# Kernel tuning notes

Hardware: AMD Instinct MI355X
Metric: run time of the kernel (lower is better)

Reference implementation:

```python
import jax, jax.numpy as jnp
import numpy as np

NUM_LAYERS = 3

def setup_inputs() -> dict:
    key = jax.random.key(0)
    ku, ki, ke1, ke2 = jax.random.split(key, 4)
    num_users, num_items, D, E = 100000, 50000, 128, 1000000
    # xavier-uniform-ish init scale for the embedding tables
    bound = float(np.sqrt(6.0 / (num_users + D)))
    user_w = jax.random.uniform(ku, (num_users, D), jnp.float32, -bound, bound)
    bound_i = float(np.sqrt(6.0 / (num_items + D)))
    item_w = jax.random.uniform(ki, (num_items, D), jnp.float32, -bound_i, bound_i)
    # bipartite edges: user -> item (item ids offset by num_users), plus reverse direction
    u = jax.random.randint(ke1, (E,), 0, num_users, dtype=jnp.int32)
    v = jax.random.randint(ke2, (E,), 0, num_items, dtype=jnp.int32) + num_users
    edge_index = jnp.stack([jnp.concatenate([u, v]), jnp.concatenate([v, u])])  # [2, 2E]
    return {"user_w": user_w, "item_w": item_w, "edge_index": edge_index,
            "num_users": num_users, "num_items": num_items}

def reference(user_w, item_w, edge_index, num_users, num_items):
    n_nodes = num_users + num_items
    src, dst = edge_index[0], edge_index[1]
    # degree via scatter-add (duplicate edges sum, same as coalesce)
    deg = jax.ops.segment_sum(jnp.ones_like(src, dtype=user_w.dtype), src,
                              num_segments=n_nodes)
    dinv = jnp.where(deg > 0, deg ** -0.5, 0.0)
    dinv = jnp.where(jnp.isfinite(dinv), dinv, 0.0)
    vals = dinv[src] * dinv[dst]  # normalized adjacency values, [2E]

    emb = jnp.concatenate([user_w, item_w], axis=0)  # [n_nodes, D]
    acc = emb
    x = emb
    for _ in range(NUM_LAYERS):
        # SpMM: out[s] += vals(e) * x[dst(e)]
        x = jax.ops.segment_sum(vals[:, None] * x[dst], src, num_segments=n_nodes)
        acc = acc + x
    final = acc / jnp.asarray(NUM_LAYERS + 1, dtype=emb.dtype)
    return final[:num_users], final[num_users:]
```

## Files before the change

kernel.cpp:

```cpp
#include <hip/hip_runtime.h>
#include <hip/hip_fp16.h>
#include <cstdint>
#include <cstddef>

#define D 128
#define BSH 9
#define BNODES 512
#define NBMAX 512
#define CCHUNK 8192
#define FP8_SCALE 2048.0f
#define FP8_INV_SCALE (1.0f / 2048.0f)

typedef float v2f __attribute__((ext_vector_type(2)));

static __device__ inline unsigned pack_fp8x4(float a, float b, float c, float d) {
    a = fminf(fmaxf(a, -440.f), 440.f);
    b = fminf(fmaxf(b, -440.f), 440.f);
    c = fminf(fmaxf(c, -440.f), 440.f);
    d = fminf(fmaxf(d, -440.f), 440.f);
    int r = 0;
    r = __builtin_amdgcn_cvt_pk_fp8_f32(a, b, r, false);
    r = __builtin_amdgcn_cvt_pk_fp8_f32(c, d, r, true);
    return (unsigned)r;
}


__global__ __launch_bounds__(256)
void k_hist_tohalf(const int* __restrict__ src, int* __restrict__ bhist,
                   int ne2, int nb, int nbh,
                   const float2* __restrict__ uw, const float2* __restrict__ iw,
                   __half2* __restrict__ x0, int nu2, int ntot2) {
    if ((int)blockIdx.x < nbh) {
        __shared__ int lc[NBMAX];
        for (int i = threadIdx.x; i < nb; i += 256) lc[i] = 0;
        __syncthreads();
        int base = blockIdx.x * CCHUNK;
        int lim = min(base + CCHUNK, ne2);
        for (int e = base + threadIdx.x; e < lim; e += 256)
            atomicAdd(&lc[src[e] >> BSH], 1);
        __syncthreads();
        for (int i = threadIdx.x; i < nb; i += 256)
            if (lc[i]) atomicAdd(&bhist[i], lc[i]);
    } else {
        int g = (blockIdx.x - nbh) * 256 + threadIdx.x;
        if (g < ntot2) {
            float2 v = (g < nu2) ? uw[g] : iw[g - nu2];
            x0[g] = __floats2half2_rn(v.x, v.y);
        }
    }
}

__global__ void k_bscan(const int* __restrict__ bhist, int* __restrict__ bbase,
                        int* __restrict__ bfill, int* __restrict__ rp,
                        int nb, int nn, int ne2) {
    __shared__ int a[NBMAX], b2[NBMAX];
    int t = threadIdx.x;
    int v = (t < nb) ? bhist[t] : 0;
    a[t] = v;
    __syncthreads();
    int* cur = a; int* nxt = b2;
    for (int o = 1; o < NBMAX; o <<= 1) {
        int x = cur[t];
        if (t >= o) x += cur[t - o];
        nxt[t] = x;
        __syncthreads();
        int* tm = cur; cur = nxt; nxt = tm;
    }
    int excl = cur[t] - v;
    if (t < nb) { bbase[t] = excl; bfill[t] = excl; }
    if (t == 0) { bbase[nb] = ne2; rp[nn] = ne2; }
}

__global__ __launch_bounds__(256)
void k_scatter(const int* __restrict__ src, const int* __restrict__ dst,
               int* __restrict__ bfill, int* __restrict__ tmp, int ne2, int nb) {
    __shared__ int lc[NBMAX], lb[NBMAX];
    for (int i = threadIdx.x; i < nb; i += 256) lc[i] = 0;
    __syncthreads();
    int base = blockIdx.x * CCHUNK;
    int rec[CCHUNK / 256];
#pragma unroll
    for (int i = 0; i < CCHUNK / 256; ++i) {
        int e = base + i * 256 + threadIdx.x;
        rec[i] = -1;
        if (e < ne2) {
            int b = src[e] >> BSH;
            int r = atomicAdd(&lc[b], 1);
            rec[i] = (r << BSH) | b;
        }
    }
    __syncthreads();
    for (int i = threadIdx.x; i < nb; i += 256)
        if (lc[i]) lb[i] = atomicAdd(&bfill[i], lc[i]);
    __syncthreads();
#pragma unroll
    for (int i = 0; i < CCHUNK / 256; ++i) {
        if (rec[i] >= 0) {
            int e = base + i * 256 + threadIdx.x;
            int b = rec[i] & (BNODES - 1);
            int r = rec[i] >> BSH;
            tmp[lb[b] + r] = ((src[e] & (BNODES - 1)) << 18) | dst[e];
        }
    }
}

__global__ __launch_bounds__(256)
void k_build(const int* __restrict__ tmp, const int* __restrict__ bbase,
             int* __restrict__ col, int* __restrict__ rp,
             float* __restrict__ dinv2, float* __restrict__ rinv,
             const float4* __restrict__ x0h, uint2* __restrict__ y0p, int nn) {
    __shared__ int cnt[BNODES];
    __shared__ int off[BNODES];
    __shared__ int wtot[4], woff[4];
    int bkt = blockIdx.x;
    int n0 = bkt << BSH;
    int nloc = min(BNODES, nn - n0);
    int ebeg = bbase[bkt], eend = bbase[bkt + 1];
    for (int i = threadIdx.x; i < BNODES; i += 256) cnt[i] = 0;
    __syncthreads();
    for (int e = ebeg + threadIdx.x; e < eend; e += 256)
        atomicAdd(&cnt[tmp[e] >> 18], 1);
    __syncthreads();
    int t = threadIdx.x;
    int c0 = cnt[2 * t], c1 = cnt[2 * t + 1];
    int s = c0 + c1;
    int lane = t & 63, wid = t >> 6;
    int x = s;
#pragma unroll
    for (int o = 1; o < 64; o <<= 1) {
        int y = __shfl_up(x, o);
        if (lane >= o) x += y;
    }
    if (lane == 63) wtot[wid] = x;
    __syncthreads();
    if (t == 0) { int a = 0; for (int k = 0; k < 4; ++k) { woff[k] = a; a += wtot[k]; } }
    __syncthreads();
    int eb = woff[wid] + x - s;
    off[2 * t] = eb;
    off[2 * t + 1] = eb + c0;
    __syncthreads();
    for (int i = threadIdx.x; i < nloc; i += 256) {
        rp[n0 + i] = ebeg + off[i];
        int c = cnt[i];
        float fc = (float)c;
        dinv2[n0 + i] = (c > 0) ? 1.0f / fc : 0.0f;
        rinv[n0 + i]  = (c > 0) ? sqrtf(fc) : 0.0f;
    }
    {
        int r = threadIdx.x >> 4;
        int l = threadIdx.x & 15;
        for (; r < nloc; r += 16) {
            int c = cnt[r];
            float sc = (c > 0) ? FP8_SCALE * rsqrtf((float)c) : 0.0f;
            float4 v = x0h[(size_t)(n0 + r) * 16 + l];
            const __half2* hp = reinterpret_cast<const __half2*>(&v);
            float2 f0 = __half22float2(hp[0]), f1 = __half22float2(hp[1]);
            float2 f2 = __half22float2(hp[2]), f3 = __half22float2(hp[3]);
            uint2 o;
            o.x = pack_fp8x4(sc * f0.x, sc * f0.y, sc * f1.x, sc * f1.y);
            o.y = pack_fp8x4(sc * f2.x, sc * f2.y, sc * f3.x, sc * f3.y);
            y0p[(size_t)(n0 + r) * 16 + l] = o;
        }
    }
    __syncthreads();
    for (int i = threadIdx.x; i < BNODES; i += 256) cnt[i] = 0;
    __syncthreads();
    for (int e = ebeg + threadIdx.x; e < eend; e += 256) {
        int v = tmp[e];
        int sl = v >> 18;
        int r = atomicAdd(&cnt[sl], 1);
        col[ebeg + off[sl] + r] = v & 0x3FFFF;
    }
}

template <int MODE>
__global__ __launch_bounds__(256)
void k_spmm(const uint2* __restrict__ yin, uint2* __restrict__ y8out,
            float4* __restrict__ h16out, const float4* __restrict__ aux1,
            const float4* __restrict__ aux2,
            const int* __restrict__ rp, const int* __restrict__ col,
            const float* __restrict__ dinv2, const float* __restrict__ rinv,
            float4* __restrict__ outp, int nn) {
    int wave = (blockIdx.x * blockDim.x + threadIdx.x) >> 6;
    int lane = threadIdx.x & 63;
    int g = lane >> 4, l16 = lane & 15;
    int node = wave * 4 + g;
    int beg = 0, end = 0;
    if (node < nn) { beg = rp[node]; end = rp[node + 1]; }
    v2f acc[4];
#pragma unroll
    for (int k = 0; k < 4; ++k) acc[k] = (v2f)(0.f);

    int srcl = g << 4;
    for (int base = beg; base < end; base += 16) {
        int p = base + l16;
        int d = (p < end) ? col[p] : 0;
        int m = min(16, end - base);
#pragma unroll 8
        for (int t = 0; t < m; ++t) {
            int dd = __shfl(d, srcl + t);
            uint2 u = yin[(size_t)dd * 16 + l16];
            acc[0] += __builtin_amdgcn_cvt_pk_f32_fp8((int)u.x, false);
            acc[1] += __builtin_amdgcn_cvt_pk_f32_fp8((int)u.x, true);
            acc[2] += __builtin_amdgcn_cvt_pk_f32_fp8((int)u.y, false);
            acc[3] += __builtin_amdgcn_cvt_pk_f32_fp8((int)u.y, true);
        }
    }
    if (node >= nn) return;
    float s2 = dinv2[node];
    size_t r16 = (size_t)node * 16 + l16;
    if (MODE != 2) {
        float yv[8];
#pragma unroll
        for (int k = 0; k < 4; ++k) {
            yv[2 * k]     = s2 * acc[k].x;
            yv[2 * k + 1] = s2 * acc[k].y;
        }
        uint2 o8;
        o8.x = pack_fp8x4(yv[0], yv[1], yv[2], yv[3]);
        o8.y = pack_fp8x4(yv[4], yv[5], yv[6], yv[7]);
        y8out[r16] = o8;
        if (MODE == 1) {
            float4 av = aux1[r16];
            const __half2* ap = reinterpret_cast<const __half2*>(&av);
#pragma unroll
            for (int k = 0; k < 4; ++k) {
                float2 fa = __half22float2(ap[k]);
                yv[2 * k]     += fa.x;
                yv[2 * k + 1] += fa.y;
            }
        }
        __half2 h[4];
#pragma unroll
        for (int k = 0; k < 4; ++k)
            h[k] = __floats2half2_rn(yv[2 * k], yv[2 * k + 1]);
        h16out[r16] = *reinterpret_cast<const float4*>(h);
    } else {
        float4 ev = aux1[r16];
        float4 zv = aux2[r16];
        const __half2* ep = reinterpret_cast<const __half2*>(&ev);
        const __half2* zp = reinterpret_cast<const __half2*>(&zv);
        float rs = rinv[node] * FP8_INV_SCALE;
        float o[8];
#pragma unroll
        for (int k = 0; k < 4; ++k) {
            float2 fe = __half22float2(ep[k]);
            float2 fz = __half22float2(zp[k]);
            o[2 * k]     = 0.25f * (fe.x + (fz.x + s2 * acc[k].x) * rs);
            o[2 * k + 1] = 0.25f * (fe.y + (fz.y + s2 * acc[k].y) * rs);
        }
        float4 w0 = make_float4(o[0], o[1], o[2], o[3]);
        float4 w1 = make_float4(o[4], o[5], o[6], o[7]);
        size_t r32 = (size_t)node * 32 + 2 * l16;
        outp[r32] = w0;
        outp[r32 + 1] = w1;
    }
}


extern "C" void kernel_launch(void* const* d_in, const int* in_sizes, int n_in,
                              void* d_out, int out_size, void* d_ws, size_t ws_size,
                              hipStream_t stream) {
    const float* uw = (const float*)d_in[0];
    const float* iw = (const float*)d_in[1];
    const int* ei = (const int*)d_in[2];

    const int NU = in_sizes[0] / D;
    const int NI = in_sizes[1] / D;
    const int NN = NU + NI;
    const int NE2 = in_sizes[2] / 2;
    const int* src = ei;
    const int* dst = ei + NE2;
    const int NB = (NN + BNODES - 1) >> BSH;

    char* p = (char*)d_ws;
    auto alloc = [&](size_t bytes) -> void* {
        void* r = (void*)p;
        p += (bytes + 255) & ~(size_t)255;
        return r;
    };
    int* bhist   = (int*)alloc(NBMAX * 4);
    int* bbase   = (int*)alloc((NBMAX + 1) * 4);
    int* bfill   = (int*)alloc(NBMAX * 4);
    int* rp      = (int*)alloc((size_t)(NN + 1) * 4);
    float* dinv2 = (float*)alloc((size_t)NN * 4);
    float* rinv  = (float*)alloc((size_t)NN * 4);
    int* col     = (int*)alloc((size_t)NE2 * 4);
    __half2* zh  = (__half2*)alloc((size_t)NN * D * 2);
    int* tmp     = (int*)zh;
    __half2* xa  = (__half2*)alloc((size_t)NN * D * 2);
    uint2* y0p   = (uint2*)alloc((size_t)NN * D);
    uint2* y1p   = (uint2*)alloc((size_t)NN * D);
    __half2* y1h = (__half2*)alloc((size_t)NN * D * 2);
    uint2* y2p   = y0p;
    float* outp  = (float*)d_out;

    hipMemsetAsync(bhist, 0, NBMAX * 4, stream);

    int ntot2 = NN * (D / 2);
    int nu2 = NU * (D / 2);
    int bce = (NE2 + CCHUNK - 1) / CCHUNK;
    int bi = (ntot2 + 255) / 256;

    k_hist_tohalf<<<bce + bi, 256, 0, stream>>>(src, bhist, NE2, NB, bce,
                                                (const float2*)uw, (const float2*)iw,
                                                xa, nu2, ntot2);
    k_bscan<<<1, NBMAX, 0, stream>>>(bhist, bbase, bfill, rp, NB, NN, NE2);
    k_scatter<<<bce, 256, 0, stream>>>(src, dst, bfill, tmp, NE2, NB);
    k_build<<<NB, 256, 0, stream>>>(tmp, bbase, col, rp, dinv2, rinv,
                                    (const float4*)xa, y0p, NN);

    int bs = (NN + 15) / 16;
    k_spmm<0><<<bs, 256, 0, stream>>>((const uint2*)y0p, y1p, (float4*)y1h,
                                      nullptr, nullptr, rp, col, dinv2, rinv,
                                      nullptr, NN);
    k_spmm<1><<<bs, 256, 0, stream>>>((const uint2*)y1p, y2p, (float4*)zh,
                                      (const float4*)y1h, nullptr, rp, col,
                                      dinv2, rinv, nullptr, NN);
    k_spmm<2><<<bs, 256, 0, stream>>>((const uint2*)y2p, nullptr, nullptr,
                                      (const float4*)xa, (const float4*)zh,
                                      rp, col, dinv2, rinv, (float4*)outp, NN);
}
```

Before: 391.9 us.

## Carry running layer sum through SpMM passes and widen build/scatter blocks

Each SpMM pass now reads the previous running sum (half precision) and writes an updated one, so every pass touches one auxiliary stream uniformly. Before, the final pass read two auxiliary arrays and the first pass read none. The y1h buffer is dropped by reusing the xa buffer. The histogram kernel uses smaller chunks so more blocks share the counting work, and the scatter and build kernels move to 512 threads so there is one thread per bucket node. The first pass now reads and writes extra data, and the rescaling changes the rounding order of the running sum.

```diff
diff --git a/kernel.cpp b/kernel.cpp
--- a/kernel.cpp
+++ b/kernel.cpp
@@ -8,6 +8,7 @@
 #define BNODES 512
 #define NBMAX 512
 #define CCHUNK 8192
+#define CCHUNK_H 2048
 #define FP8_SCALE 2048.0f
 #define FP8_INV_SCALE (1.0f / 2048.0f)
 
@@ -34,8 +35,8 @@
         __shared__ int lc[NBMAX];
         for (int i = threadIdx.x; i < nb; i += 256) lc[i] = 0;
         __syncthreads();
-        int base = blockIdx.x * CCHUNK;
-        int lim = min(base + CCHUNK, ne2);
+        int base = blockIdx.x * CCHUNK_H;
+        int lim = min(base + CCHUNK_H, ne2);
         for (int e = base + threadIdx.x; e < lim; e += 256)
             atomicAdd(&lc[src[e] >> BSH], 1);
         __syncthreads();
@@ -71,17 +72,17 @@
     if (t == 0) { bbase[nb] = ne2; rp[nn] = ne2; }
 }
 
-__global__ __launch_bounds__(256)
+__global__ __launch_bounds__(512)
 void k_scatter(const int* __restrict__ src, const int* __restrict__ dst,
                int* __restrict__ bfill, int* __restrict__ tmp, int ne2, int nb) {
     __shared__ int lc[NBMAX], lb[NBMAX];
-    for (int i = threadIdx.x; i < nb; i += 256) lc[i] = 0;
+    for (int i = threadIdx.x; i < nb; i += 512) lc[i] = 0;
     __syncthreads();
     int base = blockIdx.x * CCHUNK;
-    int rec[CCHUNK / 256];
-#pragma unroll
-    for (int i = 0; i < CCHUNK / 256; ++i) {
-        int e = base + i * 256 + threadIdx.x;
+    int rec[CCHUNK / 512];
+#pragma unroll
+    for (int i = 0; i < CCHUNK / 512; ++i) {
+        int e = base + i * 512 + threadIdx.x;
         rec[i] = -1;
         if (e < ne2) {
             int b = src[e] >> BSH;
@@ -90,13 +91,13 @@
         }
     }
     __syncthreads();
-    for (int i = threadIdx.x; i < nb; i += 256)
+    for (int i = threadIdx.x; i < nb; i += 512)
         if (lc[i]) lb[i] = atomicAdd(&bfill[i], lc[i]);
     __syncthreads();
 #pragma unroll
-    for (int i = 0; i < CCHUNK / 256; ++i) {
+    for (int i = 0; i < CCHUNK / 512; ++i) {
         if (rec[i] >= 0) {
-            int e = base + i * 256 + threadIdx.x;
+            int e = base + i * 512 + threadIdx.x;
             int b = rec[i] & (BNODES - 1);
             int r = rec[i] >> BSH;
             tmp[lb[b] + r] = ((src[e] & (BNODES - 1)) << 18) | dst[e];
@@ -104,28 +105,27 @@
     }
 }
 
-__global__ __launch_bounds__(256)
+__global__ __launch_bounds__(512)
 void k_build(const int* __restrict__ tmp, const int* __restrict__ bbase,
              int* __restrict__ col, int* __restrict__ rp,
              float* __restrict__ dinv2, float* __restrict__ rinv,
              const float4* __restrict__ x0h, uint2* __restrict__ y0p, int nn) {
     __shared__ int cnt[BNODES];
     __shared__ int off[BNODES];
-    __shared__ int wtot[4], woff[4];
+    __shared__ int wtot[8], woff[8];
     int bkt = blockIdx.x;
     int n0 = bkt << BSH;
     int nloc = min(BNODES, nn - n0);
     int ebeg = bbase[bkt], eend = bbase[bkt + 1];
-    for (int i = threadIdx.x; i < BNODES; i += 256) cnt[i] = 0;
-    __syncthreads();
-    for (int e = ebeg + threadIdx.x; e < eend; e += 256)
+    int t = threadIdx.x;
+    cnt[t] = 0;
+    __syncthreads();
+    for (int e = ebeg + t; e < eend; e += 512)
         atomicAdd(&cnt[tmp[e] >> 18], 1);
     __syncthreads();
-    int t = threadIdx.x;
-    int c0 = cnt[2 * t], c1 = cnt[2 * t + 1];
-    int s = c0 + c1;
+    int v = cnt[t];
     int lane = t & 63, wid = t >> 6;
-    int x = s;
+    int x = v;
 #pragma unroll
     for (int o = 1; o < 64; o <<= 1) {
         int y = __shfl_up(x, o);
@@ -133,27 +133,25 @@
     }
     if (lane == 63) wtot[wid] = x;
     __syncthreads();
-    if (t == 0) { int a = 0; for (int k = 0; k < 4; ++k) { woff[k] = a; a += wtot[k]; } }
-    __syncthreads();
-    int eb = woff[wid] + x - s;
-    off[2 * t] = eb;
-    off[2 * t + 1] = eb + c0;
-    __syncthreads();
-    for (int i = threadIdx.x; i < nloc; i += 256) {
-        rp[n0 + i] = ebeg + off[i];
-        int c = cnt[i];
+    if (t == 0) { int a = 0; for (int k = 0; k < 8; ++k) { woff[k] = a; a += wtot[k]; } }
+    __syncthreads();
+    off[t] = woff[wid] + x - v;
+    __syncthreads();
+    if (t < nloc) {
+        rp[n0 + t] = ebeg + off[t];
+        int c = cnt[t];
         float fc = (float)c;
-        dinv2[n0 + i] = (c > 0) ? 1.0f / fc : 0.0f;
-        rinv[n0 + i]  = (c > 0) ? sqrtf(fc) : 0.0f;
+        dinv2[n0 + t] = (c > 0) ? 1.0f / fc : 0.0f;
+        rinv[n0 + t]  = (c > 0) ? sqrtf(fc) : 0.0f;
     }
     {
-        int r = threadIdx.x >> 4;
-        int l = threadIdx.x & 15;
-        for (; r < nloc; r += 16) {
+        int r = t >> 4;
+        int l = t & 15;
+        for (; r < nloc; r += 32) {
             int c = cnt[r];
             float sc = (c > 0) ? FP8_SCALE * rsqrtf((float)c) : 0.0f;
-            float4 v = x0h[(size_t)(n0 + r) * 16 + l];
-            const __half2* hp = reinterpret_cast<const __half2*>(&v);
+            float4 fv = x0h[(size_t)(n0 + r) * 16 + l];
+            const __half2* hp = reinterpret_cast<const __half2*>(&fv);
             float2 f0 = __half22float2(hp[0]), f1 = __half22float2(hp[1]);
             float2 f2 = __half22float2(hp[2]), f3 = __half22float2(hp[3]);
             uint2 o;
@@ -163,24 +161,23 @@
         }
     }
     __syncthreads();
-    for (int i = threadIdx.x; i < BNODES; i += 256) cnt[i] = 0;
-    __syncthreads();
-    for (int e = ebeg + threadIdx.x; e < eend; e += 256) {
-        int v = tmp[e];
-        int sl = v >> 18;
+    cnt[t] = 0;
+    __syncthreads();
+    for (int e = ebeg + t; e < eend; e += 512) {
+        int pv = tmp[e];
+        int sl = pv >> 18;
         int r = atomicAdd(&cnt[sl], 1);
-        col[ebeg + off[sl] + r] = v & 0x3FFFF;
-    }
-}
-
-template <int MODE>
+        col[ebeg + off[sl] + r] = pv & 0x3FFFF;
+    }
+}
+
+template <bool FINAL>
 __global__ __launch_bounds__(256)
-void k_spmm(const uint2* __restrict__ yin, uint2* __restrict__ y8out,
-            float4* __restrict__ h16out, const float4* __restrict__ aux1,
-            const float4* __restrict__ aux2,
+void k_spmm(const uint2* __restrict__ yin, const float4* __restrict__ win,
+            uint2* __restrict__ y8out, float4* __restrict__ wout,
+            float4* __restrict__ outp,
             const int* __restrict__ rp, const int* __restrict__ col,
-            const float* __restrict__ dinv2, const float* __restrict__ rinv,
-            float4* __restrict__ outp, int nn) {
+            const float* __restrict__ dinv2, const float* __restrict__ rinv, int nn) {
     int wave = (blockIdx.x * blockDim.x + threadIdx.x) >> 6;
     int lane = threadIdx.x & 63;
     int g = lane >> 4, l16 = lane & 15;
@@ -208,49 +205,30 @@
     }
     if (node >= nn) return;
     float s2 = dinv2[node];
+    float rs = rinv[node] * FP8_INV_SCALE;
     size_t r16 = (size_t)node * 16 + l16;
-    if (MODE != 2) {
-        float yv[8];
-#pragma unroll
-        for (int k = 0; k < 4; ++k) {
-            yv[2 * k]     = s2 * acc[k].x;
-            yv[2 * k + 1] = s2 * acc[k].y;
-        }
+    float4 wv4 = win[r16];
+    const __half2* wp = reinterpret_cast<const __half2*>(&wv4);
+    float w[8];
+#pragma unroll
+    for (int k = 0; k < 4; ++k) {
+        float2 fw = __half22float2(wp[k]);
+        w[2 * k]     = fw.x + rs * (s2 * acc[k].x);
+        w[2 * k + 1] = fw.y + rs * (s2 * acc[k].y);
+    }
+    if (!FINAL) {
         uint2 o8;
-        o8.x = pack_fp8x4(yv[0], yv[1], yv[2], yv[3]);
-        o8.y = pack_fp8x4(yv[4], yv[5], yv[6], yv[7]);
+        o8.x = pack_fp8x4(s2 * acc[0].x, s2 * acc[0].y, s2 * acc[1].x, s2 * acc[1].y);
+        o8.y = pack_fp8x4(s2 * acc[2].x, s2 * acc[2].y, s2 * acc[3].x, s2 * acc[3].y);
         y8out[r16] = o8;
-        if (MODE == 1) {
-            float4 av = aux1[r16];
-            const __half2* ap = reinterpret_cast<const __half2*>(&av);
-#pragma unroll
-            for (int k = 0; k < 4; ++k) {
-                float2 fa = __half22float2(ap[k]);
-                yv[2 * k]     += fa.x;
-                yv[2 * k + 1] += fa.y;
-            }
-        }
         __half2 h[4];
 #pragma unroll
         for (int k = 0; k < 4; ++k)
-            h[k] = __floats2half2_rn(yv[2 * k], yv[2 * k + 1]);
-        h16out[r16] = *reinterpret_cast<const float4*>(h);
+            h[k] = __floats2half2_rn(w[2 * k], w[2 * k + 1]);
+        wout[r16] = *reinterpret_cast<const float4*>(h);
     } else {
-        float4 ev = aux1[r16];
-        float4 zv = aux2[r16];
-        const __half2* ep = reinterpret_cast<const __half2*>(&ev);
-        const __half2* zp = reinterpret_cast<const __half2*>(&zv);
-        float rs = rinv[node] * FP8_INV_SCALE;
-        float o[8];
-#pragma unroll
-        for (int k = 0; k < 4; ++k) {
-            float2 fe = __half22float2(ep[k]);
-            float2 fz = __half22float2(zp[k]);
-            o[2 * k]     = 0.25f * (fe.x + (fz.x + s2 * acc[k].x) * rs);
-            o[2 * k + 1] = 0.25f * (fe.y + (fz.y + s2 * acc[k].y) * rs);
-        }
-        float4 w0 = make_float4(o[0], o[1], o[2], o[3]);
-        float4 w1 = make_float4(o[4], o[5], o[6], o[7]);
+        float4 w0 = make_float4(0.25f * w[0], 0.25f * w[1], 0.25f * w[2], 0.25f * w[3]);
+        float4 w1 = make_float4(0.25f * w[4], 0.25f * w[5], 0.25f * w[6], 0.25f * w[7]);
         size_t r32 = (size_t)node * 32 + 2 * l16;
         outp[r32] = w0;
         outp[r32 + 1] = w1;
@@ -286,12 +264,12 @@
     float* dinv2 = (float*)alloc((size_t)NN * 4);
     float* rinv  = (float*)alloc((size_t)NN * 4);
     int* col     = (int*)alloc((size_t)NE2 * 4);
-    __half2* zh  = (__half2*)alloc((size_t)NN * D * 2);
-    int* tmp     = (int*)zh;
+    __half2* wh0 = (__half2*)alloc((size_t)NN * D * 2);
+    int* tmp     = (int*)wh0;
     __half2* xa  = (__half2*)alloc((size_t)NN * D * 2);
     uint2* y0p   = (uint2*)alloc((size_t)NN * D);
     uint2* y1p   = (uint2*)alloc((size_t)NN * D);
-    __half2* y1h = (__half2*)alloc((size_t)NN * D * 2);
+    __half2* wh1 = xa;
     uint2* y2p   = y0p;
     float* outp  = (float*)d_out;
 
@@ -299,25 +277,26 @@
 
     int ntot2 = NN * (D / 2);
     int nu2 = NU * (D / 2);
-    int bce = (NE2 + CCHUNK - 1) / CCHUNK;
+    int nbh = (NE2 + CCHUNK_H - 1) / CCHUNK_H;
     int bi = (ntot2 + 255) / 256;
-
-    k_hist_tohalf<<<bce + bi, 256, 0, stream>>>(src, bhist, NE2, NB, bce,
+    int bsc = (NE2 + CCHUNK - 1) / CCHUNK;
+
+    k_hist_tohalf<<<nbh + bi, 256, 0, stream>>>(src, bhist, NE2, NB, nbh,
                                                 (const float2*)uw, (const float2*)iw,
                                                 xa, nu2, ntot2);
     k_bscan<<<1, NBMAX, 0, stream>>>(bhist, bbase, bfill, rp, NB, NN, NE2);
-    k_scatter<<<bce, 256, 0, stream>>>(src, dst, bfill, tmp, NE2, NB);
-    k_build<<<NB, 256, 0, stream>>>(tmp, bbase, col, rp, dinv2, rinv,
+    k_scatter<<<bsc, 512, 0, stream>>>(src, dst, bfill, tmp, NE2, NB);
+    k_build<<<NB, 512, 0, stream>>>(tmp, bbase, col, rp, dinv2, rinv,
                                     (const float4*)xa, y0p, NN);
 
     int bs = (NN + 15) / 16;
-    k_spmm<0><<<bs, 256, 0, stream>>>((const uint2*)y0p, y1p, (float4*)y1h,
-                                      nullptr, nullptr, rp, col, dinv2, rinv,
-                                      nullptr, NN);
-    k_spmm<1><<<bs, 256, 0, stream>>>((const uint2*)y1p, y2p, (float4*)zh,
-                                      (const float4*)y1h, nullptr, rp, col,
-                                      dinv2, rinv, nullptr, NN);
-    k_spmm<2><<<bs, 256, 0, stream>>>((const uint2*)y2p, nullptr, nullptr,
-                                      (const float4*)xa, (const float4*)zh,
-                                      rp, col, dinv2, rinv, (float4*)outp, NN);
-}
+    k_spmm<false><<<bs, 256, 0, stream>>>((const uint2*)y0p, (const float4*)xa,
+                                          y1p, (float4*)wh0, nullptr,
+                                          rp, col, dinv2, rinv, NN);
+    k_spmm<false><<<bs, 256, 0, stream>>>((const uint2*)y1p, (const float4*)wh0,
+                                          y2p, (float4*)wh1, nullptr,
+                                          rp, col, dinv2, rinv, NN);
+    k_spmm<true><<<bs, 256, 0, stream>>>((const uint2*)y2p, (const float4*)wh1,
+                                         nullptr, nullptr, (float4*)outp,
+                                         rp, col, dinv2, rinv, NN);
+}
```

Result: faster. 383.6 us (-2.1%).
